# Optimization experiments

Measured on AMD Instinct MI355X. Metric: run time of the kernel, lower is better.

Reference implementation:

```python
import jax, jax.numpy as jnp
import numpy as np

N, E, DIM, H = 50000, 800000, 256, 4
HD = DIM // H  # per-head dim = 64
NEG_SLOPE = 0.2
EPS = 1e-5


def _layernorm(x, g, b):
    mu = jnp.mean(x, axis=-1, keepdims=True)
    var = jnp.mean(jnp.square(x - mu), axis=-1, keepdims=True)
    return (x - mu) * jax.lax.rsqrt(var + EPS) * g + b


def setup_inputs() -> dict:
    key = jax.random.key(0)
    ks = jax.random.split(key, 8)
    s = 1.0 / np.sqrt(DIM)
    return {
        "x": jax.random.normal(ks[0], (N, DIM), dtype=jnp.float32),
        "edge_index": jax.random.randint(ks[1], (2, E), 0, N, dtype=jnp.int64),
        "W": jax.random.normal(ks[2], (DIM, DIM), dtype=jnp.float32) * s,
        "a_src": jax.random.normal(ks[3], (H, HD), dtype=jnp.float32) * s,
        "a_dst": jax.random.normal(ks[4], (H, HD), dtype=jnp.float32) * s,
        "gat_b": jnp.zeros((DIM,), jnp.float32),
        "ln1_g": jnp.ones((DIM,), jnp.float32),
        "ln1_b": jnp.zeros((DIM,), jnp.float32),
        "W1": jax.random.normal(ks[5], (DIM, 2 * DIM), dtype=jnp.float32) * s,
        "b1": jnp.zeros((2 * DIM,), jnp.float32),
        "W2": jax.random.normal(ks[6], (2 * DIM, DIM), dtype=jnp.float32) * (1.0 / np.sqrt(2 * DIM)),
        "b2": jnp.zeros((DIM,), jnp.float32),
        "ln2_g": jnp.ones((DIM,), jnp.float32),
        "ln2_b": jnp.zeros((DIM,), jnp.float32),
    }


def _gat(x, edge_index, W, a_src, a_dst, gat_b):
    # add self-loops (PyG GATConv default)
    loops = jnp.arange(N, dtype=edge_index.dtype)
    src = jnp.concatenate([edge_index[0], loops])
    dst = jnp.concatenate([edge_index[1], loops])
    h = (x @ W).reshape(N, H, HD)                    # [N,H,D]
    al_src = jnp.einsum("nhd,hd->nh", h, a_src)      # [N,H]
    al_dst = jnp.einsum("nhd,hd->nh", h, a_dst)
    e = jax.nn.leaky_relu(al_src[src] + al_dst[dst], NEG_SLOPE)  # [E',H]
    # softmax over edges grouped by destination node
    emax = jax.ops.segment_max(e, dst, num_segments=N)           # [N,H]
    ex = jnp.exp(e - emax[dst])
    denom = jax.ops.segment_sum(ex, dst, num_segments=N)         # [N,H]
    alpha = ex / denom[dst]                                      # [E',H]
    msg = alpha[:, :, None] * h[src]                             # [E',H,D]
    out = jax.ops.segment_sum(msg, dst, num_segments=N)          # [N,H,D]
    return out.reshape(N, DIM) + gat_b


def reference(x, edge_index, W, a_src, a_dst, gat_b, ln1_g, ln1_b, W1, b1, W2, b2, ln2_g, ln2_b):
    res = x
    y = _gat(x, edge_index, W, a_src, a_dst, gat_b)
    y = _layernorm(y + res, ln1_g, ln1_b)
    res = y
    f = jax.nn.gelu(y @ W1 + b1, approximate=False) @ W2 + b2
    return _layernorm(f + res, ln2_g, ln2_b)
```

## Files before the change

### kernel.cpp

```cpp
#include <hip/hip_runtime.h>

typedef __bf16 bf16_t;
typedef __bf16 bf16x4 __attribute__((ext_vector_type(4)));
typedef __bf16 bf16x8 __attribute__((ext_vector_type(8)));
typedef float  f32x4  __attribute__((ext_vector_type(4)));
typedef unsigned u32x2 __attribute__((ext_vector_type(2)));

__device__ inline float loadf(const void* p, size_t i, int bf) {
    return bf ? (float)((const bf16_t*)p)[i] : ((const float*)p)[i];
}
__device__ inline void storef(void* p, size_t i, int bf, float v) {
    if (bf) ((bf16_t*)p)[i] = (bf16_t)v; else ((float*)p)[i] = v;
}
__device__ inline int eidx(const void* p, size_t i, int i64) {
    return i64 ? (int)((const long long*)p)[i] : ((const int*)p)[i];
}
__device__ inline float bflo(unsigned u) { return __uint_as_float(u << 16); }
__device__ inline float bfhi(unsigned u) { return __uint_as_float(u & 0xFFFF0000u); }

__device__ inline void gload16(const bf16_t* g, char* l) {
    __builtin_amdgcn_global_load_lds(
        (const __attribute__((address_space(1))) unsigned*)g,
        (__attribute__((address_space(3))) unsigned*)l, 16, 0, 0);
}

__global__ void detect_k(const void* __restrict__ x, const void* __restrict__ ei,
                         int E, int* __restrict__ flags) {
    int l = threadIdx.x;
    const unsigned* xu = (const unsigned*)x;
    unsigned low = xu[l] & 0xFFFFu;
    unsigned ex = (low >> 7) & 0xFF;
    int cnt = __popcll(__ballot(ex >= 115 && ex <= 133));
    const unsigned* eu = (const unsigned*)ei;
    int lim = E < 64 ? E : 64;
    unsigned v = (l < lim) ? eu[2 * (size_t)l + 1] : 0u;
    unsigned long long nz = __ballot(v != 0u);
    if (l == 0) { flags[0] = (cnt >= 32) ? 1 : 0; flags[1] = (nz == 0ull) ? 1 : 0; }
}

__global__ void tobf16_k(const void* __restrict__ in, bf16_t* __restrict__ out,
                         long n, const int* __restrict__ flags) {
    int bf = flags[0];
    long i = ((long)blockIdx.x * 256 + threadIdx.x) * 8;
    long stride = (long)gridDim.x * 256 * 8;
    if (bf) {
        for (; i < n; i += stride)
            *(bf16x8*)&out[i] = *(const bf16x8*)((const bf16_t*)in + i);
    } else {
        for (; i < n; i += stride) {
            f32x4 a = *(const f32x4*)((const float*)in + i);
            f32x4 b = *(const f32x4*)((const float*)in + i + 4);
            bf16x8 r;
            r[0]=(bf16_t)a[0]; r[1]=(bf16_t)a[1]; r[2]=(bf16_t)a[2]; r[3]=(bf16_t)a[3];
            r[4]=(bf16_t)b[0]; r[5]=(bf16_t)b[1]; r[6]=(bf16_t)b[2]; r[7]=(bf16_t)b[3];
            *(bf16x8*)&out[i] = r;
        }
    }
}

__global__ void transpose_k(const void* __restrict__ in, bf16_t* __restrict__ out,
                            int R, int C, const int* __restrict__ flags) {
    int bf = flags[0];
    int i = blockIdx.x * 256 + threadIdx.x;
    if (i < R * C) { int r = i / C, c = i % C; out[c * R + r] = (bf16_t)loadf(in, i, bf); }
}

__global__ __launch_bounds__(256) void gemm128(const bf16_t* __restrict__ A,
                                               const bf16_t* __restrict__ BT,
                                               const void* __restrict__ bias,
                                               bf16_t* __restrict__ C,
                                               int M, int N, int K, int act,
                                               const int* __restrict__ flags,
                                               const void* __restrict__ a_srcp,
                                               const void* __restrict__ a_dstp,
                                               float* __restrict__ alsrc,
                                               float* __restrict__ aldst, int do_al) {
    int bf = flags[0];
    __shared__ __align__(16) char smem[34816];
    int t = threadIdx.x;
    int tm = blockIdx.x * 128;
    int tn = blockIdx.y * 128;
    int w = t >> 6, l = t & 63;
    int wr = (w >> 1) * 64, wc = (w & 1) * 64;
    int lr16 = l & 15, kg = l >> 4;
    int NK = K >> 5;

    f32x4 acc[4][4];
#pragma unroll
    for (int i = 0; i < 4; i++)
#pragma unroll
        for (int j = 0; j < 4; j++) acc[i][j] = (f32x4){0.f, 0.f, 0.f, 0.f};

    bool fast = (tm + 128 <= M);

    if (fast) {
        int buf = 0;
#pragma unroll
        for (int ii = 0; ii < 2; ii++) {
            int c = w + ii * 4;
            int rowa = tm + (c & 1) * 64 + l;
            int rowb = tn + (c & 1) * 64 + l;
            int kc = (c >> 1) * 8;
            gload16(A  + (size_t)rowa * K + kc, smem +         c * 1024 + l * 16);
            gload16(BT + (size_t)rowb * K + kc, smem + 16384 + c * 1024 + l * 16);
        }
        __syncthreads();
        for (int ks = 0; ks < NK; ks++) {
            if (ks + 1 < NK) {
                int k0 = (ks + 1) << 5;
                char* ab = smem + (buf ^ 1) * 8192;
                char* bb = smem + 16384 + (buf ^ 1) * 8192;
#pragma unroll
                for (int ii = 0; ii < 2; ii++) {
                    int c = w + ii * 4;
                    int rowa = tm + (c & 1) * 64 + l;
                    int rowb = tn + (c & 1) * 64 + l;
                    int kc = k0 + (c >> 1) * 8;
                    gload16(A  + (size_t)rowa * K + kc, ab + c * 1024 + l * 16);
                    gload16(BT + (size_t)rowb * K + kc, bb + c * 1024 + l * 16);
                }
            }
            const char* ab = smem + buf * 8192;
            const char* bb = smem + 16384 + buf * 8192;
            bf16x8 af[4], bg[4];
#pragma unroll
            for (int i = 0; i < 4; i++) {
                af[i] = *(const bf16x8*)(ab + ((size_t)(kg * 128 + wr + i * 16 + lr16)) * 16);
                bg[i] = *(const bf16x8*)(bb + ((size_t)(kg * 128 + wc + i * 16 + lr16)) * 16);
            }
#pragma unroll
            for (int i = 0; i < 4; i++)
#pragma unroll
                for (int j = 0; j < 4; j++)
                    acc[i][j] = __builtin_amdgcn_mfma_f32_16x16x32_bf16(af[i], bg[j], acc[i][j], 0, 0, 0);
            __syncthreads();
            buf ^= 1;
        }
    } else {
        int r = t >> 2, kg2 = t & 3;
        for (int ks = 0; ks < NK; ks++) {
            int k0 = ks << 5;
            bf16x8 va[2], vb[2];
#pragma unroll
            for (int j = 0; j < 2; j++) {
                int row = r + j * 64;
                int ra = tm + row; if (ra > M - 1) ra = M - 1;
                va[j] = *(const bf16x8*)(A + (size_t)ra * K + k0 + kg2 * 8);
                vb[j] = *(const bf16x8*)(BT + (size_t)(tn + row) * K + k0 + kg2 * 8);
            }
            __syncthreads();
#pragma unroll
            for (int j = 0; j < 2; j++) {
                int row = r + j * 64;
                *(bf16x8*)(smem + ((size_t)(kg2 * 128 + row)) * 16) = va[j];
                *(bf16x8*)(smem + 16384 + ((size_t)(kg2 * 128 + row)) * 16) = vb[j];
            }
            __syncthreads();
            bf16x8 af[4], bg[4];
#pragma unroll
            for (int i = 0; i < 4; i++) {
                af[i] = *(const bf16x8*)(smem + ((size_t)(kg * 128 + wr + i * 16 + lr16)) * 16);
                bg[i] = *(const bf16x8*)(smem + 16384 + ((size_t)(kg * 128 + wc + i * 16 + lr16)) * 16);
            }
#pragma unroll
            for (int i = 0; i < 4; i++)
#pragma unroll
                for (int j = 0; j < 4; j++)
                    acc[i][j] = __builtin_amdgcn_mfma_f32_16x16x32_bf16(af[i], bg[j], acc[i][j], 0, 0, 0);
        }
        __syncthreads();
    }

    int cr0 = (l >> 4) * 4;

    if (do_al) {
        float asv[4], adv[4];
#pragma unroll
        for (int j = 0; j < 4; j++) {
            int col = tn + wc + j * 16 + lr16;
            asv[j] = loadf(a_srcp, col, bf);
            adv[j] = loadf(a_dstp, col, bf);
        }
        int head = (tn + wc) >> 6;
#pragma unroll
        for (int i = 0; i < 4; i++) {
#pragma unroll
            for (int q = 0; q < 4; q++) {
                float ps = acc[i][0][q]*asv[0] + acc[i][1][q]*asv[1] + acc[i][2][q]*asv[2] + acc[i][3][q]*asv[3];
                float pd = acc[i][0][q]*adv[0] + acc[i][1][q]*adv[1] + acc[i][2][q]*adv[2] + acc[i][3][q]*adv[3];
#pragma unroll
                for (int d = 1; d < 16; d <<= 1) { ps += __shfl_xor(ps, d); pd += __shfl_xor(pd, d); }
                int row = tm + wr + i * 16 + cr0 + q;
                if (lr16 == 0 && row < M) { alsrc[row * 4 + head] = ps; aldst[row * 4 + head] = pd; }
            }
        }
    }

    bf16_t (*Cst)[136] = (bf16_t(*)[136])smem;
#pragma unroll
    for (int i = 0; i < 4; i++) {
#pragma unroll
        for (int j = 0; j < 4; j++) {
            int col = wc + j * 16 + lr16;
            float bv = bias ? loadf(bias, tn + col, bf) : 0.f;
#pragma unroll
            for (int q = 0; q < 4; q++) {
                float v = acc[i][j][q] + bv;
                if (act) v = 0.5f * v * (1.f + erff(v * 0.70710678118f));
                Cst[wr + i * 16 + cr0 + q][col] = (bf16_t)v;
            }
        }
    }
    __syncthreads();
#pragma unroll
    for (int it = 0; it < 8; it++) {
        int idx = it * 256 + t;
        int row = idx >> 4;
        int c8 = (idx & 15) * 8;
        if (tm + row < M)
            *(bf16x8*)&C[(size_t)(tm + row) * N + tn + c8] = *(const bf16x8*)&Cst[row][c8];
    }
}

__global__ void deg_k(const void* __restrict__ ei, int* __restrict__ deg, int E, int N,
                      const int* __restrict__ flags) {
    int i64 = flags[1];
    int i = blockIdx.x * 256 + threadIdx.x;
    if (i < E) {
        int d = eidx(ei, (size_t)E + i, i64);
        if ((unsigned)d >= (unsigned)N) d = 0;
        atomicAdd(&deg[d], 1);
    }
}

__global__ __launch_bounds__(256) void scan1(const int* __restrict__ deg, int* __restrict__ offs,
                                             int* __restrict__ chunkSum) {
    __shared__ int s[256];
    int t = threadIdx.x, b = blockIdx.x;
    int v = deg[b * 256 + t];
    s[t] = v; __syncthreads();
#pragma unroll
    for (int d = 1; d < 256; d <<= 1) {
        int u = (t >= d) ? s[t - d] : 0;
        __syncthreads(); s[t] += u; __syncthreads();
    }
    offs[b * 256 + t] = s[t] - v;
    if (t == 255) chunkSum[b] = s[255];
}

__global__ __launch_bounds__(256) void scan2(const int* __restrict__ chunkSum, int* __restrict__ chunkOff, int nch) {
    __shared__ int s[256];
    int t = threadIdx.x;
    int v = (t < nch) ? chunkSum[t] : 0;
    s[t] = v; __syncthreads();
#pragma unroll
    for (int d = 1; d < 256; d <<= 1) {
        int u = (t >= d) ? s[t - d] : 0;
        __syncthreads(); s[t] += u; __syncthreads();
    }
    chunkOff[t] = s[t] - v;
}

__global__ void scan3(int* __restrict__ offs, const int* __restrict__ chunkOff,
                      int* __restrict__ cursor, int total) {
    int i = blockIdx.x * 256 + threadIdx.x;
    if (i < total) { int v = offs[i] + chunkOff[i >> 8]; offs[i] = v; cursor[i] = v; }
}

__global__ void scatter_k(const void* __restrict__ ei, int* __restrict__ cursor,
                          int* __restrict__ csr, bf16_t* __restrict__ ewsb,
                          const float* __restrict__ alsrc, const float* __restrict__ aldst,
                          int E, int N, const int* __restrict__ flags) {
    int i64 = flags[1];
    int i = blockIdx.x * 256 + threadIdx.x;
    if (i < E) {
        int s = eidx(ei, i, i64);
        int d = eidx(ei, (size_t)E + i, i64);
        if ((unsigned)s >= (unsigned)N) s = 0;
        if ((unsigned)d >= (unsigned)N) d = 0;
        int p = atomicAdd(&cursor[d], 1);
        csr[p] = s;
        f32x4 as4 = *(const f32x4*)&alsrc[s * 4];
        f32x4 ad4 = *(const f32x4*)&aldst[d * 4];
        bf16x4 w4;
#pragma unroll
        for (int hh = 0; hh < 4; hh++) {
            float e = as4[hh] + ad4[hh];
            e = e > 0.f ? e : 0.2f * e;
            w4[hh] = (bf16_t)expf(fminf(e, 30.f));
        }
        *(bf16x4*)&ewsb[4 * (size_t)p] = w4;
    }
}

__global__ __launch_bounds__(256) void gat_agg_ln(
    const bf16_t* __restrict__ hbuf, const void* __restrict__ x,
    const float* __restrict__ alsrc, const float* __restrict__ aldst,
    const int* __restrict__ offs, const int* __restrict__ csr,
    const bf16_t* __restrict__ ewsb,
    const void* __restrict__ gatb, const void* __restrict__ lng, const void* __restrict__ lnb,
    bf16_t* __restrict__ y, const int* __restrict__ flags, int N) {
    int bf = flags[0];
    int w = threadIdx.x >> 6, l = threadIdx.x & 63;
    int n = blockIdx.x * 4 + w;
    if (n >= N) return;
    int h = l >> 4;
    int col0 = l * 4;

    __shared__ int   srcs[4][64];
    __shared__ float ewt[4][4][68];

    int off = offs[n], deg = offs[n + 1] - off;

    float es = alsrc[n * 4 + h] + aldst[n * 4 + h];
    es = es > 0.f ? es : 0.2f * es;
    float wself = expf(fminf(es, 30.f));

    float a0 = 0.f, a1 = 0.f, a2 = 0.f, a3 = 0.f;
    f32x4 ssum = (f32x4){0.f, 0.f, 0.f, 0.f};

    for (int c0 = 0; c0 < deg; c0 += 64) {
        int cl = deg - c0; if (cl > 64) cl = 64;
        if (l < cl) {
            int sv = csr[off + c0 + l];
            srcs[w][l] = sv;
            bf16x4 wv4 = *(const bf16x4*)&ewsb[4 * (size_t)(off + c0 + l)];
            float w0 = (float)wv4[0], w1 = (float)wv4[1], w2 = (float)wv4[2], w3 = (float)wv4[3];
            ewt[w][0][l] = w0; ewt[w][1][l] = w1;
            ewt[w][2][l] = w2; ewt[w][3][l] = w3;
            ssum += (f32x4){w0, w1, w2, w3};
        }
        int i = 0;
        for (; i + 4 <= cl; i += 4) {
            int s0 = __builtin_amdgcn_readfirstlane(srcs[w][i]);
            int s1 = __builtin_amdgcn_readfirstlane(srcs[w][i + 1]);
            int s2 = __builtin_amdgcn_readfirstlane(srcs[w][i + 2]);
            int s3 = __builtin_amdgcn_readfirstlane(srcs[w][i + 3]);
            u32x2 v0 = ((const u32x2*)(hbuf + (size_t)s0 * 256))[l];
            u32x2 v1 = ((const u32x2*)(hbuf + (size_t)s1 * 256))[l];
            u32x2 v2 = ((const u32x2*)(hbuf + (size_t)s2 * 256))[l];
            u32x2 v3 = ((const u32x2*)(hbuf + (size_t)s3 * 256))[l];
            f32x4 wq = *(const f32x4*)&ewt[w][h][i];
            a0 += wq[0]*bflo(v0[0]); a1 += wq[0]*bfhi(v0[0]); a2 += wq[0]*bflo(v0[1]); a3 += wq[0]*bfhi(v0[1]);
            a0 += wq[1]*bflo(v1[0]); a1 += wq[1]*bfhi(v1[0]); a2 += wq[1]*bflo(v1[1]); a3 += wq[1]*bfhi(v1[1]);
            a0 += wq[2]*bflo(v2[0]); a1 += wq[2]*bfhi(v2[0]); a2 += wq[2]*bflo(v2[1]); a3 += wq[2]*bfhi(v2[1]);
            a0 += wq[3]*bflo(v3[0]); a1 += wq[3]*bfhi(v3[0]); a2 += wq[3]*bflo(v3[1]); a3 += wq[3]*bfhi(v3[1]);
        }
        for (; i < cl; i++) {
            int sv = __builtin_amdgcn_readfirstlane(srcs[w][i]);
            float wgt = ewt[w][h][i];
            u32x2 v0 = ((const u32x2*)(hbuf + (size_t)sv * 256))[l];
            a0 += wgt*bflo(v0[0]); a1 += wgt*bfhi(v0[0]); a2 += wgt*bflo(v0[1]); a3 += wgt*bfhi(v0[1]);
        }
    }

#pragma unroll
    for (int d = 1; d < 64; d <<= 1) {
        ssum[0] += __shfl_xor(ssum[0], d);
        ssum[1] += __shfl_xor(ssum[1], d);
        ssum[2] += __shfl_xor(ssum[2], d);
        ssum[3] += __shfl_xor(ssum[3], d);
    }
    float dsum = (h == 0) ? ssum[0] : (h == 1) ? ssum[1] : (h == 2) ? ssum[2] : ssum[3];
    float di = 1.f / (dsum + wself);

    u32x2 sv2 = ((const u32x2*)(hbuf + (size_t)n * 256))[l];
    size_t xbase = (size_t)n * 256 + col0;
    float v0f = (a0 + wself*bflo(sv2[0])) * di + loadf(gatb, col0 + 0, bf) + loadf(x, xbase + 0, bf);
    float v1f = (a1 + wself*bfhi(sv2[0])) * di + loadf(gatb, col0 + 1, bf) + loadf(x, xbase + 1, bf);
    float v2f = (a2 + wself*bflo(sv2[1])) * di + loadf(gatb, col0 + 2, bf) + loadf(x, xbase + 2, bf);
    float v3f = (a3 + wself*bfhi(sv2[1])) * di + loadf(gatb, col0 + 3, bf) + loadf(x, xbase + 3, bf);

    float s1 = v0f + v1f + v2f + v3f;
#pragma unroll
    for (int d = 1; d < 64; d <<= 1) s1 += __shfl_xor(s1, d);
    float mu = s1 * (1.f / 256.f);
    float c0f = v0f - mu, c1f = v1f - mu, c2f = v2f - mu, c3f = v3f - mu;
    float sq = c0f*c0f + c1f*c1f + c2f*c2f + c3f*c3f;
#pragma unroll
    for (int d = 1; d < 64; d <<= 1) sq += __shfl_xor(sq, d);
    float rs = rsqrtf(sq * (1.f / 256.f) + 1e-5f);

    bf16x4 o;
    o[0] = (bf16_t)(c0f * rs * loadf(lng, col0 + 0, bf) + loadf(lnb, col0 + 0, bf));
    o[1] = (bf16_t)(c1f * rs * loadf(lng, col0 + 1, bf) + loadf(lnb, col0 + 1, bf));
    o[2] = (bf16_t)(c2f * rs * loadf(lng, col0 + 2, bf) + loadf(lnb, col0 + 2, bf));
    o[3] = (bf16_t)(c3f * rs * loadf(lng, col0 + 3, bf) + loadf(lnb, col0 + 3, bf));
    *(bf16x4*)&y[(size_t)n * 256 + col0] = o;
}

__global__ __launch_bounds__(256) void ln_res(const bf16_t* __restrict__ f, const bf16_t* __restrict__ y,
                                              const void* __restrict__ g, const void* __restrict__ b,
                                              void* __restrict__ out, int N, const int* __restrict__ flags) {
    int bf = flags[0];
    int row = blockIdx.x * 4 + (threadIdx.x >> 6);
    int l = threadIdx.x & 63;
    if (row >= N) return;
    int col0 = l * 4;
    u32x2 fv = *(const u32x2*)(f + (size_t)row * 256 + col0);
    u32x2 yv = *(const u32x2*)(y + (size_t)row * 256 + col0);
    float v0 = bflo(fv[0]) + bflo(yv[0]);
    float v1 = bfhi(fv[0]) + bfhi(yv[0]);
    float v2 = bflo(fv[1]) + bflo(yv[1]);
    float v3 = bfhi(fv[1]) + bfhi(yv[1]);
    float s = v0 + v1 + v2 + v3;
#pragma unroll
    for (int d = 1; d < 64; d <<= 1) s += __shfl_xor(s, d);
    float mu = s * (1.f / 256.f);
    float c0 = v0 - mu, c1 = v1 - mu, c2 = v2 - mu, c3 = v3 - mu;
    float sq = c0*c0 + c1*c1 + c2*c2 + c3*c3;
#pragma unroll
    for (int d = 1; d < 64; d <<= 1) sq += __shfl_xor(sq, d);
    float rs = rsqrtf(sq * (1.f / 256.f) + 1e-5f);
    float o0 = c0 * rs * loadf(g, col0 + 0, bf) + loadf(b, col0 + 0, bf);
    float o1 = c1 * rs * loadf(g, col0 + 1, bf) + loadf(b, col0 + 1, bf);
    float o2 = c2 * rs * loadf(g, col0 + 2, bf) + loadf(b, col0 + 2, bf);
    float o3 = c3 * rs * loadf(g, col0 + 3, bf) + loadf(b, col0 + 3, bf);
    if (bf) {
        bf16x4 o; o[0]=(bf16_t)o0; o[1]=(bf16_t)o1; o[2]=(bf16_t)o2; o[3]=(bf16_t)o3;
        *(bf16x4*)&((bf16_t*)out)[(size_t)row * 256 + col0] = o;
    } else {
        f32x4 o = (f32x4){o0, o1, o2, o3};
        *(f32x4*)&((float*)out)[(size_t)row * 256 + col0] = o;
    }
}

extern "C" void kernel_launch(void* const* d_in, const int* in_sizes, int n_in,
                              void* d_out, int out_size, void* d_ws, size_t ws_size,
                              hipStream_t stream) {
    const void* x    = d_in[0];
    const void* ei   = d_in[1];
    const void* W    = d_in[2];
    const void* a_src= d_in[3];
    const void* a_dst= d_in[4];
    const void* gatb = d_in[5];
    const void* ln1g = d_in[6];
    const void* ln1b = d_in[7];
    const void* W1   = d_in[8];
    const void* b1   = d_in[9];
    const void* W2   = d_in[10];
    const void* b2   = d_in[11];
    const void* ln2g = d_in[12];
    const void* ln2b = d_in[13];

    const int DIM = 256, DFF = 512;
    int N = in_sizes[0] / DIM;
    int E = in_sizes[1] / 2;

    char* ws = (char*)d_ws;
    size_t o = 0;
    auto alloc = [&](size_t bytes) { void* p = ws + o; o += (bytes + 255) & ~(size_t)255; return p; };
    int*    flags  = (int*)alloc(256);
    bf16_t* WT     = (bf16_t*)alloc((size_t)DIM * DIM * 2);
    bf16_t* W1T    = (bf16_t*)alloc((size_t)DIM * DFF * 2);
    bf16_t* W2T    = (bf16_t*)alloc((size_t)DFF * DIM * 2);
    float*  alsrc  = (float*)alloc((size_t)N * 4 * 4);
    float*  aldst  = (float*)alloc((size_t)N * 4 * 4);
    int nch = (N + 255) / 256;
    int tot = nch * 256;
    int* deg      = (int*)alloc((size_t)tot * 4);
    int* offs     = (int*)alloc((size_t)(tot + 1) * 4);
    int* cursor   = (int*)alloc((size_t)tot * 4);
    int* chunkSum = (int*)alloc(256 * 4);
    int* chunkOff = (int*)alloc(256 * 4);
    int* csr      = (int*)alloc((size_t)E * 4);
    bf16_t* ewsb  = (bf16_t*)alloc((size_t)E * 8);
    bf16_t* h     = (bf16_t*)alloc((size_t)N * DIM * 2);
    bf16_t* yb    = (bf16_t*)alloc((size_t)N * DIM * 2);
    bf16_t* xb    = (bf16_t*)alloc((size_t)N * DIM * 2);
    bf16_t* fb    = h;
    size_t remain = (ws_size > o) ? (ws_size - o) : 0;
    long CH = (long)(remain / ((size_t)DFF * 2));
    if (CH > N) CH = N;
    if (CH < 1024) CH = 1024;
    bf16_t* t1 = (bf16_t*)alloc((size_t)CH * DFF * 2);

    detect_k<<<1, 64, 0, stream>>>(x, ei, E, flags);
    hipMemsetAsync(deg, 0, (size_t)tot * 4, stream);

    tobf16_k<<<4096, 256, 0, stream>>>(x, xb, (long)N * DIM, flags);
    transpose_k<<<(DIM * DIM + 255) / 256, 256, 0, stream>>>(W,  WT,  DIM, DIM, flags);
    transpose_k<<<(DIM * DFF + 255) / 256, 256, 0, stream>>>(W1, W1T, DIM, DFF, flags);
    transpose_k<<<(DFF * DIM + 255) / 256, 256, 0, stream>>>(W2, W2T, DFF, DIM, flags);

    dim3 g1((N + 127) / 128, DIM / 128);
    gemm128<<<g1, 256, 0, stream>>>(xb, WT, nullptr, h, N, DIM, DIM, 0, flags,
                                    a_src, a_dst, alsrc, aldst, 1);

    deg_k<<<(E + 255) / 256, 256, 0, stream>>>(ei, deg, E, N, flags);
    scan1<<<nch, 256, 0, stream>>>(deg, offs, chunkSum);
    scan2<<<1, 256, 0, stream>>>(chunkSum, chunkOff, nch);
    scan3<<<(tot + 255) / 256, 256, 0, stream>>>(offs, chunkOff, cursor, tot);
    scatter_k<<<(E + 255) / 256, 256, 0, stream>>>(ei, cursor, csr, ewsb, alsrc, aldst, E, N, flags);

    gat_agg_ln<<<(N + 3) / 4, 256, 0, stream>>>(h, x, alsrc, aldst, offs, csr, ewsb,
                                                gatb, ln1g, ln1b, yb, flags, N);

    for (long r0 = 0; r0 < N; r0 += CH) {
        int m = (int)((N - r0 < CH) ? (N - r0) : CH);
        dim3 g2((m + 127) / 128, DFF / 128);
        gemm128<<<g2, 256, 0, stream>>>(yb + r0 * DIM, W1T, b1, t1, m, DFF, DIM, 1, flags,
                                        nullptr, nullptr, nullptr, nullptr, 0);
        dim3 g3((m + 127) / 128, DIM / 128);
        gemm128<<<g3, 256, 0, stream>>>(t1, W2T, b2, fb + r0 * DIM, m, DIM, DFF, 0, flags,
                                        nullptr, nullptr, nullptr, nullptr, 0);
    }

    ln_res<<<(N + 3) / 4, 256, 0, stream>>>(fb, yb, ln2g, ln2b, d_out, N, flags);
}
```

Measured before the change: 366.3 us.

## Fuse FFN GEMMs, GELU, bias and LayerNorm into one kernel; unroll aggregation by 8

```diff
diff --git a/kernel.cpp b/kernel.cpp
--- a/kernel.cpp
+++ b/kernel.cpp
@@ -8,9 +8,6 @@
 
 __device__ inline float loadf(const void* p, size_t i, int bf) {
     return bf ? (float)((const bf16_t*)p)[i] : ((const float*)p)[i];
-}
-__device__ inline void storef(void* p, size_t i, int bf, float v) {
-    if (bf) ((bf16_t*)p)[i] = (bf16_t)v; else ((float*)p)[i] = v;
 }
 __device__ inline int eidx(const void* p, size_t i, int i64) {
     return i64 ? (int)((const long long*)p)[i] : ((const int*)p)[i];
@@ -67,14 +64,13 @@
 
 __global__ __launch_bounds__(256) void gemm128(const bf16_t* __restrict__ A,
                                                const bf16_t* __restrict__ BT,
-                                               const void* __restrict__ bias,
                                                bf16_t* __restrict__ C,
-                                               int M, int N, int K, int act,
+                                               int M, int N, int K,
                                                const int* __restrict__ flags,
                                                const void* __restrict__ a_srcp,
                                                const void* __restrict__ a_dstp,
                                                float* __restrict__ alsrc,
-                                               float* __restrict__ aldst, int do_al) {
+                                               float* __restrict__ aldst) {
     int bf = flags[0];
     __shared__ __align__(16) char smem[34816];
     int t = threadIdx.x;
@@ -171,9 +167,9 @@
         __syncthreads();
     }
 
-    int cr0 = (l >> 4) * 4;
-
-    if (do_al) {
+    int cr0 = kg * 4;
+
+    {
         float asv[4], adv[4];
 #pragma unroll
         for (int j = 0; j < 4; j++) {
@@ -202,13 +198,9 @@
 #pragma unroll
         for (int j = 0; j < 4; j++) {
             int col = wc + j * 16 + lr16;
-            float bv = bias ? loadf(bias, tn + col, bf) : 0.f;
-#pragma unroll
-            for (int q = 0; q < 4; q++) {
-                float v = acc[i][j][q] + bv;
-                if (act) v = 0.5f * v * (1.f + erff(v * 0.70710678118f));
-                Cst[wr + i * 16 + cr0 + q][col] = (bf16_t)v;
-            }
+#pragma unroll
+            for (int q = 0; q < 4; q++)
+                Cst[wr + i * 16 + cr0 + q][col] = (bf16_t)acc[i][j][q];
         }
     }
     __syncthreads();
@@ -331,6 +323,22 @@
             ssum += (f32x4){w0, w1, w2, w3};
         }
         int i = 0;
+        for (; i + 8 <= cl; i += 8) {
+            int sv[8]; u32x2 vv[8];
+#pragma unroll
+            for (int k = 0; k < 8; k++) sv[k] = __builtin_amdgcn_readfirstlane(srcs[w][i + k]);
+#pragma unroll
+            for (int k = 0; k < 8; k++) vv[k] = ((const u32x2*)(hbuf + (size_t)sv[k] * 256))[l];
+            f32x4 wqa = *(const f32x4*)&ewt[w][h][i];
+            f32x4 wqb = *(const f32x4*)&ewt[w][h][i + 4];
+#pragma unroll
+            for (int k = 0; k < 4; k++) {
+                a0 += wqa[k]*bflo(vv[k][0]); a1 += wqa[k]*bfhi(vv[k][0]);
+                a2 += wqa[k]*bflo(vv[k][1]); a3 += wqa[k]*bfhi(vv[k][1]);
+                a0 += wqb[k]*bflo(vv[k+4][0]); a1 += wqb[k]*bfhi(vv[k+4][0]);
+                a2 += wqb[k]*bflo(vv[k+4][1]); a3 += wqb[k]*bfhi(vv[k+4][1]);
+            }
+        }
         for (; i + 4 <= cl; i += 4) {
             int s0 = __builtin_amdgcn_readfirstlane(srcs[w][i]);
             int s1 = __builtin_amdgcn_readfirstlane(srcs[w][i + 1]);
@@ -389,39 +397,135 @@
     *(bf16x4*)&y[(size_t)n * 256 + col0] = o;
 }
 
-__global__ __launch_bounds__(256) void ln_res(const bf16_t* __restrict__ f, const bf16_t* __restrict__ y,
-                                              const void* __restrict__ g, const void* __restrict__ b,
-                                              void* __restrict__ out, int N, const int* __restrict__ flags) {
+__global__ __launch_bounds__(512) void ffn_fused(
+    const bf16_t* __restrict__ yb, const bf16_t* __restrict__ W1T,
+    const void* __restrict__ b1, const bf16_t* __restrict__ W2T,
+    const void* __restrict__ b2, const void* __restrict__ lng,
+    const void* __restrict__ lnb, void* __restrict__ out,
+    int N, const int* __restrict__ flags) {
     int bf = flags[0];
-    int row = blockIdx.x * 4 + (threadIdx.x >> 6);
-    int l = threadIdx.x & 63;
-    if (row >= N) return;
+    __shared__ __align__(16) char fsm[65536];
+    int t = threadIdx.x;
+    int w = t >> 6, l = t & 63;
+    int lr16 = l & 15, kg = l >> 4;
+    int cr0 = kg * 4;
+    int r0 = blockIdx.x * 64;
+
+    {
+        int WC = w * 64;
+        f32x4 acc[4][4];
+#pragma unroll
+        for (int i = 0; i < 4; i++)
+#pragma unroll
+            for (int j = 0; j < 4; j++) acc[i][j] = (f32x4){0.f, 0.f, 0.f, 0.f};
+        for (int ks = 0; ks < 8; ks++) {
+            int kc = ks * 32 + kg * 8;
+            bf16x8 af[4], bg[4];
+#pragma unroll
+            for (int i = 0; i < 4; i++) {
+                int row = r0 + i * 16 + lr16; if (row > N - 1) row = N - 1;
+                af[i] = *(const bf16x8*)(yb + (size_t)row * 256 + kc);
+            }
+#pragma unroll
+            for (int j = 0; j < 4; j++)
+                bg[j] = *(const bf16x8*)(W1T + (size_t)(WC + j * 16 + lr16) * 256 + kc);
+#pragma unroll
+            for (int i = 0; i < 4; i++)
+#pragma unroll
+                for (int j = 0; j < 4; j++)
+                    acc[i][j] = __builtin_amdgcn_mfma_f32_16x16x32_bf16(af[i], bg[j], acc[i][j], 0, 0, 0);
+        }
+#pragma unroll
+        for (int i = 0; i < 4; i++) {
+#pragma unroll
+            for (int j = 0; j < 4; j++) {
+                int col = WC + j * 16 + lr16;
+                float bv = loadf(b1, col, bf);
+#pragma unroll
+                for (int q = 0; q < 4; q++) {
+                    int row = i * 16 + cr0 + q;
+                    float v = acc[i][j][q] + bv;
+                    v = 0.5f * v * (1.f + erff(v * 0.70710678118f));
+                    int byte = row * 1024 + ((col * 2) ^ ((row & 7) << 4));
+                    *(bf16_t*)(fsm + byte) = (bf16_t)v;
+                }
+            }
+        }
+    }
+    __syncthreads();
+
+    int wr2 = (w >> 2) * 32, wc2 = (w & 3) * 64;
+    f32x4 acc2[2][4];
+#pragma unroll
+    for (int i = 0; i < 2; i++)
+#pragma unroll
+        for (int j = 0; j < 4; j++) acc2[i][j] = (f32x4){0.f, 0.f, 0.f, 0.f};
+    for (int ks = 0; ks < 16; ks++) {
+        int kc = ks * 32 + kg * 8;
+        bf16x8 af2[2], bg2[4];
+#pragma unroll
+        for (int i = 0; i < 2; i++) {
+            int row = wr2 + i * 16 + lr16;
+            int byte = row * 1024 + ((kc * 2) ^ ((row & 7) << 4));
+            af2[i] = *(const bf16x8*)(fsm + byte);
+        }
+#pragma unroll
+        for (int j = 0; j < 4; j++)
+            bg2[j] = *(const bf16x8*)(W2T + (size_t)(wc2 + j * 16 + lr16) * 512 + kc);
+#pragma unroll
+        for (int i = 0; i < 2; i++)
+#pragma unroll
+            for (int j = 0; j < 4; j++)
+                acc2[i][j] = __builtin_amdgcn_mfma_f32_16x16x32_bf16(af2[i], bg2[j], acc2[i][j], 0, 0, 0);
+    }
+    __syncthreads();
+
+    bf16_t (*Cst)[264] = (bf16_t(*)[264])fsm;
+#pragma unroll
+    for (int i = 0; i < 2; i++) {
+#pragma unroll
+        for (int j = 0; j < 4; j++) {
+            int col = wc2 + j * 16 + lr16;
+            float bv = loadf(b2, col, bf);
+#pragma unroll
+            for (int q = 0; q < 4; q++)
+                Cst[wr2 + i * 16 + cr0 + q][col] = (bf16_t)(acc2[i][j][q] + bv);
+        }
+    }
+    __syncthreads();
+
     int col0 = l * 4;
-    u32x2 fv = *(const u32x2*)(f + (size_t)row * 256 + col0);
-    u32x2 yv = *(const u32x2*)(y + (size_t)row * 256 + col0);
-    float v0 = bflo(fv[0]) + bflo(yv[0]);
-    float v1 = bfhi(fv[0]) + bfhi(yv[0]);
-    float v2 = bflo(fv[1]) + bflo(yv[1]);
-    float v3 = bfhi(fv[1]) + bfhi(yv[1]);
-    float s = v0 + v1 + v2 + v3;
-#pragma unroll
-    for (int d = 1; d < 64; d <<= 1) s += __shfl_xor(s, d);
-    float mu = s * (1.f / 256.f);
-    float c0 = v0 - mu, c1 = v1 - mu, c2 = v2 - mu, c3 = v3 - mu;
-    float sq = c0*c0 + c1*c1 + c2*c2 + c3*c3;
-#pragma unroll
-    for (int d = 1; d < 64; d <<= 1) sq += __shfl_xor(sq, d);
-    float rs = rsqrtf(sq * (1.f / 256.f) + 1e-5f);
-    float o0 = c0 * rs * loadf(g, col0 + 0, bf) + loadf(b, col0 + 0, bf);
-    float o1 = c1 * rs * loadf(g, col0 + 1, bf) + loadf(b, col0 + 1, bf);
-    float o2 = c2 * rs * loadf(g, col0 + 2, bf) + loadf(b, col0 + 2, bf);
-    float o3 = c3 * rs * loadf(g, col0 + 3, bf) + loadf(b, col0 + 3, bf);
-    if (bf) {
-        bf16x4 o; o[0]=(bf16_t)o0; o[1]=(bf16_t)o1; o[2]=(bf16_t)o2; o[3]=(bf16_t)o3;
-        *(bf16x4*)&((bf16_t*)out)[(size_t)row * 256 + col0] = o;
-    } else {
-        f32x4 o = (f32x4){o0, o1, o2, o3};
-        *(f32x4*)&((float*)out)[(size_t)row * 256 + col0] = o;
+#pragma unroll
+    for (int r = 0; r < 8; r++) {
+        int rl = w * 8 + r;
+        int g = r0 + rl;
+        if (g >= N) break;
+        bf16x4 cv = *(const bf16x4*)&Cst[rl][col0];
+        u32x2 yv = *(const u32x2*)(yb + (size_t)g * 256 + col0);
+        float v0 = (float)cv[0] + bflo(yv[0]);
+        float v1 = (float)cv[1] + bfhi(yv[0]);
+        float v2 = (float)cv[2] + bflo(yv[1]);
+        float v3 = (float)cv[3] + bfhi(yv[1]);
+        float s = v0 + v1 + v2 + v3;
+#pragma unroll
+        for (int d = 1; d < 64; d <<= 1) s += __shfl_xor(s, d);
+        float mu = s * (1.f / 256.f);
+        float c0 = v0 - mu, c1 = v1 - mu, c2 = v2 - mu, c3 = v3 - mu;
+        float sq = c0*c0 + c1*c1 + c2*c2 + c3*c3;
+#pragma unroll
+        for (int d = 1; d < 64; d <<= 1) sq += __shfl_xor(sq, d);
+        float rs = rsqrtf(sq * (1.f / 256.f) + 1e-5f);
+        float o0 = c0 * rs * loadf(lng, col0 + 0, bf) + loadf(lnb, col0 + 0, bf);
+        float o1 = c1 * rs * loadf(lng, col0 + 1, bf) + loadf(lnb, col0 + 1, bf);
+        float o2 = c2 * rs * loadf(lng, col0 + 2, bf) + loadf(lnb, col0 + 2, bf);
+        float o3 = c3 * rs * loadf(lng, col0 + 3, bf) + loadf(lnb, col0 + 3, bf);
+        if (bf) {
+            bf16x4 o; o[0]=(bf16_t)o0; o[1]=(bf16_t)o1; o[2]=(bf16_t)o2; o[3]=(bf16_t)o3;
+            *(bf16x4*)&((bf16_t*)out)[(size_t)g * 256 + col0] = o;
+        } else {
+            f32x4 o = (f32x4){o0, o1, o2, o3};
+            *(f32x4*)&((float*)out)[(size_t)g * 256 + col0] = o;
+        }
     }
 }
 
@@ -468,12 +572,6 @@
     bf16_t* h     = (bf16_t*)alloc((size_t)N * DIM * 2);
     bf16_t* yb    = (bf16_t*)alloc((size_t)N * DIM * 2);
     bf16_t* xb    = (bf16_t*)alloc((size_t)N * DIM * 2);
-    bf16_t* fb    = h;
-    size_t remain = (ws_size > o) ? (ws_size - o) : 0;
-    long CH = (long)(remain / ((size_t)DFF * 2));
-    if (CH > N) CH = N;
-    if (CH < 1024) CH = 1024;
-    bf16_t* t1 = (bf16_t*)alloc((size_t)CH * DFF * 2);
 
     detect_k<<<1, 64, 0, stream>>>(x, ei, E, flags);
     hipMemsetAsync(deg, 0, (size_t)tot * 4, stream);
@@ -484,8 +582,8 @@
     transpose_k<<<(DFF * DIM + 255) / 256, 256, 0, stream>>>(W2, W2T, DFF, DIM, flags);
 
     dim3 g1((N + 127) / 128, DIM / 128);
-    gemm128<<<g1, 256, 0, stream>>>(xb, WT, nullptr, h, N, DIM, DIM, 0, flags,
-                                    a_src, a_dst, alsrc, aldst, 1);
+    gemm128<<<g1, 256, 0, stream>>>(xb, WT, h, N, DIM, DIM, flags,
+                                    a_src, a_dst, alsrc, aldst);
 
     deg_k<<<(E + 255) / 256, 256, 0, stream>>>(ei, deg, E, N, flags);
     scan1<<<nch, 256, 0, stream>>>(deg, offs, chunkSum);
@@ -496,15 +594,6 @@
     gat_agg_ln<<<(N + 3) / 4, 256, 0, stream>>>(h, x, alsrc, aldst, offs, csr, ewsb,
                                                 gatb, ln1g, ln1b, yb, flags, N);
 
-    for (long r0 = 0; r0 < N; r0 += CH) {
-        int m = (int)((N - r0 < CH) ? (N - r0) : CH);
-        dim3 g2((m + 127) / 128, DFF / 128);
-        gemm128<<<g2, 256, 0, stream>>>(yb + r0 * DIM, W1T, b1, t1, m, DFF, DIM, 1, flags,
-                                        nullptr, nullptr, nullptr, nullptr, 0);
-        dim3 g3((m + 127) / 128, DIM / 128);
-        gemm128<<<g3, 256, 0, stream>>>(t1, W2T, b2, fb + r0 * DIM, m, DIM, DFF, 0, flags,
-                                        nullptr, nullptr, nullptr, nullptr, 0);
-    }
-
-    ln_res<<<(N + 3) / 4, 256, 0, stream>>>(fb, yb, ln2g, ln2b, d_out, N, flags);
-}
+    ffn_fused<<<(N + 63) / 64, 512, 0, stream>>>(yb, W1T, b1, W2T, b2, ln2g, ln2b,
+                                                 d_out, N, flags);
+}
```

Result: slower. 444.8 us (+21.4%).

## Fuse second FFN GEMM with bias, residual and LayerNorm; unroll gather by 8

Applied to the files above, without the earlier changes.

```diff
diff --git a/kernel.cpp b/kernel.cpp
--- a/kernel.cpp
+++ b/kernel.cpp
@@ -8,9 +8,6 @@
 
 __device__ inline float loadf(const void* p, size_t i, int bf) {
     return bf ? (float)((const bf16_t*)p)[i] : ((const float*)p)[i];
-}
-__device__ inline void storef(void* p, size_t i, int bf, float v) {
-    if (bf) ((bf16_t*)p)[i] = (bf16_t)v; else ((float*)p)[i] = v;
 }
 __device__ inline int eidx(const void* p, size_t i, int i64) {
     return i64 ? (int)((const long long*)p)[i] : ((const int*)p)[i];
@@ -171,7 +168,7 @@
         __syncthreads();
     }
 
-    int cr0 = (l >> 4) * 4;
+    int cr0 = kg * 4;
 
     if (do_al) {
         float asv[4], adv[4];
@@ -219,6 +216,120 @@
         int c8 = (idx & 15) * 8;
         if (tm + row < M)
             *(bf16x8*)&C[(size_t)(tm + row) * N + tn + c8] = *(const bf16x8*)&Cst[row][c8];
+    }
+}
+
+__global__ __launch_bounds__(256) void ffn3(const bf16_t* __restrict__ T1,
+                                            const bf16_t* __restrict__ W2T,
+                                            const void* __restrict__ b2,
+                                            const bf16_t* __restrict__ ybc,
+                                            const void* __restrict__ lng,
+                                            const void* __restrict__ lnb,
+                                            void* __restrict__ out, long orow0,
+                                            int M, const int* __restrict__ flags) {
+    int bf = flags[0];
+    __shared__ __align__(16) char smem[40960];
+    int t = threadIdx.x;
+    int tm = blockIdx.x * 64;
+    int w = t >> 6, l = t & 63;
+    int wr = (w >> 1) * 32, wc = (w & 1) * 128;
+    int lr16 = l & 15, kg = l >> 4;
+    const int K = 512, NK = 16;
+
+    f32x4 acc[2][8];
+#pragma unroll
+    for (int i = 0; i < 2; i++)
+#pragma unroll
+        for (int j = 0; j < 8; j++) acc[i][j] = (f32x4){0.f, 0.f, 0.f, 0.f};
+
+    int ra = tm + l; if (ra > M - 1) ra = M - 1;
+
+    {
+        gload16(T1 + (size_t)ra * K + w * 8, smem + w * 1024 + l * 16);
+#pragma unroll
+        for (int rr = 0; rr < 4; rr++)
+            gload16(W2T + (size_t)(rr * 64 + l) * K + w * 8,
+                    smem + 8192 + w * 4096 + rr * 1024 + l * 16);
+    }
+    __syncthreads();
+    int buf = 0;
+    for (int ks = 0; ks < NK; ks++) {
+        if (ks + 1 < NK) {
+            int kc = ((ks + 1) << 5) + w * 8;
+            char* ab = smem + (buf ^ 1) * 4096;
+            char* bb = smem + 8192 + (buf ^ 1) * 16384;
+            gload16(T1 + (size_t)ra * K + kc, ab + w * 1024 + l * 16);
+#pragma unroll
+            for (int rr = 0; rr < 4; rr++)
+                gload16(W2T + (size_t)(rr * 64 + l) * K + kc,
+                        bb + w * 4096 + rr * 1024 + l * 16);
+        }
+        const char* ab = smem + buf * 4096;
+        const char* bb = smem + 8192 + buf * 16384;
+        bf16x8 af[2], bg[8];
+#pragma unroll
+        for (int i = 0; i < 2; i++)
+            af[i] = *(const bf16x8*)(ab + ((size_t)(kg * 1024) + (wr + i * 16 + lr16) * 16));
+#pragma unroll
+        for (int j = 0; j < 8; j++)
+            bg[j] = *(const bf16x8*)(bb + ((size_t)(kg * 4096) + (wc + j * 16 + lr16) * 16));
+#pragma unroll
+        for (int i = 0; i < 2; i++)
+#pragma unroll
+            for (int j = 0; j < 8; j++)
+                acc[i][j] = __builtin_amdgcn_mfma_f32_16x16x32_bf16(af[i], bg[j], acc[i][j], 0, 0, 0);
+        __syncthreads();
+        buf ^= 1;
+    }
+
+    bf16_t (*Cst)[264] = (bf16_t(*)[264])smem;
+    int cr0 = kg * 4;
+#pragma unroll
+    for (int i = 0; i < 2; i++) {
+#pragma unroll
+        for (int j = 0; j < 8; j++) {
+            int col = wc + j * 16 + lr16;
+            float bv = loadf(b2, col, bf);
+#pragma unroll
+            for (int q = 0; q < 4; q++)
+                Cst[wr + i * 16 + cr0 + q][col] = (bf16_t)(acc[i][j][q] + bv);
+        }
+    }
+    __syncthreads();
+
+    int col0 = l * 4;
+#pragma unroll
+    for (int r = 0; r < 16; r++) {
+        int row = w * 16 + r;
+        int g = tm + row;
+        if (g >= M) break;
+        bf16x4 cv = *(const bf16x4*)&Cst[row][col0];
+        u32x2 yv = *(const u32x2*)(ybc + (size_t)g * 256 + col0);
+        float v0 = (float)cv[0] + bflo(yv[0]);
+        float v1 = (float)cv[1] + bfhi(yv[0]);
+        float v2 = (float)cv[2] + bflo(yv[1]);
+        float v3 = (float)cv[3] + bfhi(yv[1]);
+        float s = v0 + v1 + v2 + v3;
+#pragma unroll
+        for (int d = 1; d < 64; d <<= 1) s += __shfl_xor(s, d);
+        float mu = s * (1.f / 256.f);
+        float c0 = v0 - mu, c1 = v1 - mu, c2 = v2 - mu, c3 = v3 - mu;
+        float sq = c0*c0 + c1*c1 + c2*c2 + c3*c3;
+#pragma unroll
+        for (int d = 1; d < 64; d <<= 1) sq += __shfl_xor(sq, d);
+        float rs = rsqrtf(sq * (1.f / 256.f) + 1e-5f);
+        float o0 = c0 * rs * loadf(lng, col0 + 0, bf) + loadf(lnb, col0 + 0, bf);
+        float o1 = c1 * rs * loadf(lng, col0 + 1, bf) + loadf(lnb, col0 + 1, bf);
+        float o2 = c2 * rs * loadf(lng, col0 + 2, bf) + loadf(lnb, col0 + 2, bf);
+        float o3 = c3 * rs * loadf(lng, col0 + 3, bf) + loadf(lnb, col0 + 3, bf);
+        size_t obase = (size_t)(orow0 + g) * 256 + col0;
+        if (bf) {
+            bf16x4 o; o[0]=(bf16_t)o0; o[1]=(bf16_t)o1; o[2]=(bf16_t)o2; o[3]=(bf16_t)o3;
+            *(bf16x4*)&((bf16_t*)out)[obase] = o;
+        } else {
+            f32x4 o = (f32x4){o0, o1, o2, o3};
+            *(f32x4*)&((float*)out)[obase] = o;
+        }
     }
 }
 
@@ -331,6 +442,22 @@
             ssum += (f32x4){w0, w1, w2, w3};
         }
         int i = 0;
+        for (; i + 8 <= cl; i += 8) {
+            int sv[8]; u32x2 vv[8];
+#pragma unroll
+            for (int k = 0; k < 8; k++) sv[k] = __builtin_amdgcn_readfirstlane(srcs[w][i + k]);
+#pragma unroll
+            for (int k = 0; k < 8; k++) vv[k] = ((const u32x2*)(hbuf + (size_t)sv[k] * 256))[l];
+            f32x4 wqa = *(const f32x4*)&ewt[w][h][i];
+            f32x4 wqb = *(const f32x4*)&ewt[w][h][i + 4];
+#pragma unroll
+            for (int k = 0; k < 4; k++) {
+                a0 += wqa[k]*bflo(vv[k][0]); a1 += wqa[k]*bfhi(vv[k][0]);
+                a2 += wqa[k]*bflo(vv[k][1]); a3 += wqa[k]*bfhi(vv[k][1]);
+                a0 += wqb[k]*bflo(vv[k+4][0]); a1 += wqb[k]*bfhi(vv[k+4][0]);
+                a2 += wqb[k]*bflo(vv[k+4][1]); a3 += wqb[k]*bfhi(vv[k+4][1]);
+            }
+        }
         for (; i + 4 <= cl; i += 4) {
             int s0 = __builtin_amdgcn_readfirstlane(srcs[w][i]);
             int s1 = __builtin_amdgcn_readfirstlane(srcs[w][i + 1]);
@@ -387,42 +514,6 @@
     o[2] = (bf16_t)(c2f * rs * loadf(lng, col0 + 2, bf) + loadf(lnb, col0 + 2, bf));
     o[3] = (bf16_t)(c3f * rs * loadf(lng, col0 + 3, bf) + loadf(lnb, col0 + 3, bf));
     *(bf16x4*)&y[(size_t)n * 256 + col0] = o;
-}
-
-__global__ __launch_bounds__(256) void ln_res(const bf16_t* __restrict__ f, const bf16_t* __restrict__ y,
-                                              const void* __restrict__ g, const void* __restrict__ b,
-                                              void* __restrict__ out, int N, const int* __restrict__ flags) {
-    int bf = flags[0];
-    int row = blockIdx.x * 4 + (threadIdx.x >> 6);
-    int l = threadIdx.x & 63;
-    if (row >= N) return;
-    int col0 = l * 4;
-    u32x2 fv = *(const u32x2*)(f + (size_t)row * 256 + col0);
-    u32x2 yv = *(const u32x2*)(y + (size_t)row * 256 + col0);
-    float v0 = bflo(fv[0]) + bflo(yv[0]);
-    float v1 = bfhi(fv[0]) + bfhi(yv[0]);
-    float v2 = bflo(fv[1]) + bflo(yv[1]);
-    float v3 = bfhi(fv[1]) + bfhi(yv[1]);
-    float s = v0 + v1 + v2 + v3;
-#pragma unroll
-    for (int d = 1; d < 64; d <<= 1) s += __shfl_xor(s, d);
-    float mu = s * (1.f / 256.f);
-    float c0 = v0 - mu, c1 = v1 - mu, c2 = v2 - mu, c3 = v3 - mu;
-    float sq = c0*c0 + c1*c1 + c2*c2 + c3*c3;
-#pragma unroll
-    for (int d = 1; d < 64; d <<= 1) sq += __shfl_xor(sq, d);
-    float rs = rsqrtf(sq * (1.f / 256.f) + 1e-5f);
-    float o0 = c0 * rs * loadf(g, col0 + 0, bf) + loadf(b, col0 + 0, bf);
-    float o1 = c1 * rs * loadf(g, col0 + 1, bf) + loadf(b, col0 + 1, bf);
-    float o2 = c2 * rs * loadf(g, col0 + 2, bf) + loadf(b, col0 + 2, bf);
-    float o3 = c3 * rs * loadf(g, col0 + 3, bf) + loadf(b, col0 + 3, bf);
-    if (bf) {
-        bf16x4 o; o[0]=(bf16_t)o0; o[1]=(bf16_t)o1; o[2]=(bf16_t)o2; o[3]=(bf16_t)o3;
-        *(bf16x4*)&((bf16_t*)out)[(size_t)row * 256 + col0] = o;
-    } else {
-        f32x4 o = (f32x4){o0, o1, o2, o3};
-        *(f32x4*)&((float*)out)[(size_t)row * 256 + col0] = o;
-    }
 }
 
 extern "C" void kernel_launch(void* const* d_in, const int* in_sizes, int n_in,
@@ -468,11 +559,11 @@
     bf16_t* h     = (bf16_t*)alloc((size_t)N * DIM * 2);
     bf16_t* yb    = (bf16_t*)alloc((size_t)N * DIM * 2);
     bf16_t* xb    = (bf16_t*)alloc((size_t)N * DIM * 2);
-    bf16_t* fb    = h;
     size_t remain = (ws_size > o) ? (ws_size - o) : 0;
     long CH = (long)(remain / ((size_t)DFF * 2));
     if (CH > N) CH = N;
     if (CH < 1024) CH = 1024;
+    CH &= ~63L;
     bf16_t* t1 = (bf16_t*)alloc((size_t)CH * DFF * 2);
 
     detect_k<<<1, 64, 0, stream>>>(x, ei, E, flags);
@@ -501,10 +592,7 @@
         dim3 g2((m + 127) / 128, DFF / 128);
         gemm128<<<g2, 256, 0, stream>>>(yb + r0 * DIM, W1T, b1, t1, m, DFF, DIM, 1, flags,
                                         nullptr, nullptr, nullptr, nullptr, 0);
-        dim3 g3((m + 127) / 128, DIM / 128);
-        gemm128<<<g3, 256, 0, stream>>>(t1, W2T, b2, fb + r0 * DIM, m, DIM, DFF, 0, flags,
-                                        nullptr, nullptr, nullptr, nullptr, 0);
-    }
-
-    ln_res<<<(N + 3) / 4, 256, 0, stream>>>(fb, yb, ln2g, ln2b, d_out, N, flags);
-}
+        ffn3<<<(m + 63) / 64, 256, 0, stream>>>(t1, W2T, b2, yb + r0 * DIM, ln2g, ln2b,
+                                                d_out, r0, m, flags);
+    }
+}
```

Result: slower. 435.7 us (+18.9%).
